# Performance work log

Measured on AMD Instinct MI355X. Metric: run time of the kernel, lower is better.

Reference implementation:

```python
import jax, jax.numpy as jnp
import numpy as np

INPUT_SIZE = 512.0
NMS_THRESH = 0.3
SCORE_THRESH = 0.5
TOPC = 256        # candidates entering NMS (top-scoring above-threshold boxes)
MAX_DETS = 32     # py_cpu_nms(...)[:32]


def conv3x3(x, w):
    return jax.lax.conv_general_dilated(x, w, (1, 1), 'SAME',
                                        dimension_numbers=('NCHW', 'OIHW', 'NCHW'))


def bn_eval(x, g, b, m, v, eps=1e-5):
    inv = g * jax.lax.rsqrt(v + eps)
    return x * inv[None, :, None, None] + (b - m * inv)[None, :, None, None]


def lrelu(x):
    return jnp.where(x >= 0, x, 0.01 * x)


def upsample2x(x):  # F.interpolate(scale_factor=2), default nearest
    return jnp.repeat(jnp.repeat(x, 2, axis=2), 2, axis=3)


def fpn_head(x, hw1, hg1, hb1, hm1, hv1, hw2, hg2, hb2, hm2, hv2):
    x = lrelu(bn_eval(conv3x3(x, hw1), hg1, hb1, hm1, hv1))
    x = lrelu(bn_eval(conv3x3(x, hw2), hg2, hb2, hm2, hv2))
    return x


def decode_boxes(t, a):
    # inverse of coordinate_change: x1 = ax1 + tx*aw, w = aw*exp(tw)
    aw = a[:, 2] - a[:, 0]
    ah = a[:, 3] - a[:, 1]
    x1 = a[:, 0] + t[:, 0] * aw
    y1 = a[:, 1] + t[:, 1] * ah
    bw = aw * jnp.exp(t[:, 2])
    bh = ah * jnp.exp(t[:, 3])
    return jnp.stack([x1, y1, x1 + bw, y1 + bh], axis=1)


def pairwise_iou_p1(b):
    # py_cpu_nms convention: +1 in widths/areas
    x1, y1, x2, y2 = b[:, 0], b[:, 1], b[:, 2], b[:, 3]
    areas = (x2 - x1 + 1.0) * (y2 - y1 + 1.0)
    xx1 = jnp.maximum(x1[:, None], x1[None, :])
    yy1 = jnp.maximum(y1[:, None], y1[None, :])
    xx2 = jnp.minimum(x2[:, None], x2[None, :])
    yy2 = jnp.minimum(y2[:, None], y2[None, :])
    inter = jnp.maximum(0.0, xx2 - xx1 + 1.0) * jnp.maximum(0.0, yy2 - yy1 + 1.0)
    return inter / (areas[:, None] + areas[None, :] - inter)


def nms_keep(boxes, valid):
    # boxes pre-sorted by descending score; greedy suppression
    ovr = pairwise_iou_p1(boxes)
    idxs = jnp.arange(boxes.shape[0])

    def body(i, keep):
        sup = (ovr[i] > NMS_THRESH) & (idxs > i) & keep[i]
        return keep & ~sup

    return jax.lax.fori_loop(0, boxes.shape[0], body, valid)


def roi_adaptive_maxpool(feat, c):
    # feat [C,h,w]; c = [x1,y1,x2,y2] int32 feature-map coords
    # faithful F.adaptive_max_pool2d(feat[:, y1:y2, x1:x2], (7,7))
    C, h, w = feat.shape
    neg = jnp.finfo(feat.dtype).min

    def bin_masks(lo, hi, n_axis):
        L = hi - lo
        i = jnp.arange(7)
        start = (i * L) // 7
        end = ((i + 1) * L + 6) // 7  # ceil
        rel = jnp.arange(n_axis) - lo
        return (rel[None, :] >= start[:, None]) & (rel[None, :] < end[:, None])

    my = bin_masks(c[1], c[3], h)  # [7,h]
    mx = bin_masks(c[0], c[2], w)  # [7,w]
    rows = jnp.stack([jnp.max(jnp.where(my[i][None, :, None], feat, neg), axis=1)
                      for i in range(7)])                    # [7y,C,w]
    cols = jnp.stack([jnp.max(jnp.where(mx[j][None, None, :], rows, neg), axis=2)
                      for j in range(7)])
    return cols.transpose(2, 1, 0)


def rpn_level(feat, anchors, stride, clsw, locw):
    B = feat.shape[0]
    score = jax.nn.sigmoid(conv3x3(feat, clsw)).transpose(0, 2, 3, 1).reshape(B, -1)
    loc = conv3x3(feat, locw).transpose(0, 2, 3, 1).reshape(B, -1, 4)

    def per_image(f, sc, t):
        boxes = jnp.clip(decode_boxes(t, anchors), 0.0, INPUT_SIZE)
        bw = boxes[:, 2] - boxes[:, 0]
        bh = boxes[:, 3] - boxes[:, 1]
        valid = (sc > SCORE_THRESH) & (bw >= 2.0 * stride) & (bh >= 2.0 * stride)
        vals, idx = jax.lax.top_k(jnp.where(valid, sc, -1.0), TOPC)
        cb = boxes[idx]
        # original NMS ran on detached numpy -> stop_gradient
        keep = nms_keep(jax.lax.stop_gradient(cb), vals > SCORE_THRESH)
        order = jnp.argsort(jnp.where(keep, 0, 1), stable=True)[:MAX_DETS]
        m = keep[order]
        b32 = cb[order]
        s32 = vals[order]
        coords = jnp.where(m[:, None], b32.astype(jnp.int32) // stride,
                           jnp.array([0, 0, 2, 2], jnp.int32))
        pooled = jax.vmap(lambda cc: roi_adaptive_maxpool(f, cc))(coords)
        pooled = jnp.where(m[:, None, None, None], pooled, 0.0)
        dets = jnp.where(m[:, None], jnp.concatenate([b32, s32[:, None]], axis=1), 0.0)
        return dets, m, pooled

    return jax.vmap(per_image)(feat, score, loc)


def net_forward(layer2, layer3, layer4, anchors2, anchors3, anchors4,
                hw1, hg1, hb1, hm1, hv1, hw2, hg2, hb2, hm2, hv2, clsw, locw):
    head = (hw1, hg1, hb1, hm1, hv1, hw2, hg2, hb2, hm2, hv2)
    l3 = layer3 + upsample2x(layer4)
    l2 = layer2 + upsample2x(l3)
    f2 = fpn_head(l2, *head)
    f3 = fpn_head(l3, *head)
    f4 = fpn_head(layer4, *head)
    outs = [rpn_level(f, a, s, clsw, locw)
            for f, a, s in ((f2, anchors2, 8), (f3, anchors3, 16), (f4, anchors4, 32))]
    dets = jnp.stack([o[0] for o in outs], axis=1)  # [B,3,32,5] padded eval_test
    mask = jnp.stack([o[1] for o in outs], axis=1)  # [B,3,32] validity of each det
    rois = jnp.stack([o[2] for o in outs], axis=1)  # [B,3,32,256,7,7]
    return dets, mask, rois


def setup_inputs() -> dict:
    key = jax.random.key(0)
    ks = jax.random.split(key, 16)
    f32 = jnp.float32

    def n(k, shape, s=1.0):
        return jax.random.normal(k, shape, f32) * s

    S = 512

    def anchors_for(st):
        h = S // st
        c = (jnp.arange(h, dtype=f32) + 0.5) * st
        sz = jnp.array([4.0, 6.0, 8.0], f32) * st
        cy = jnp.broadcast_to(c[:, None, None], (h, h, 3))
        cx = jnp.broadcast_to(c[None, :, None], (h, h, 3))
        ss = jnp.broadcast_to(sz[None, None, :], (h, h, 3))
        return jnp.stack([cx - ss / 2, cy - ss / 2, cx + ss / 2, cy + ss / 2], -1).reshape(-1, 4)

    return {
        'layer2': n(ks[0], (2, 256, 64, 64)),
        'layer3': n(ks[1], (2, 256, 32, 32)),
        'layer4': n(ks[2], (2, 256, 16, 16)),
        'anchors2': anchors_for(8),
        'anchors3': anchors_for(16),
        'anchors4': anchors_for(32),
        'hw1': n(ks[3], (256, 256, 3, 3), 0.03),
        'hg1': 1.0 + n(ks[4], (256,), 0.1),
        'hb1': n(ks[5], (256,), 0.1),
        'hm1': n(ks[6], (256,), 0.1),
        'hv1': jax.random.uniform(ks[7], (256,), f32, 0.5, 1.5),
        'hw2': n(ks[8], (256, 256, 3, 3), 0.03),
        'hg2': 1.0 + n(ks[9], (256,), 0.1),
        'hb2': n(ks[10], (256,), 0.1),
        'hm2': n(ks[11], (256,), 0.1),
        'hv2': jax.random.uniform(ks[12], (256,), f32, 0.5, 1.5),
        'clsw': n(ks[13], (3, 256, 3, 3), 0.03),
        'locw': n(ks[14], (12, 256, 3, 3), 0.01),
    }


def reference(layer2, layer3, layer4, anchors2, anchors3, anchors4,
              hw1, hg1, hb1, hm1, hv1, hw2, hg2, hb2, hm2, hv2, clsw, locw):
    return net_forward(layer2, layer3, layer4, anchors2, anchors3, anchors4,
                       hw1, hg1, hb1, hm1, hv1, hw2, hg2, hb2, hm2, hv2, clsw, locw)
```

## Files before the change

kernel.cpp:

```cpp
#include <hip/hip_runtime.h>
#include <math.h>

typedef __attribute__((ext_vector_type(8))) _Float16 f16x8;
typedef __attribute__((ext_vector_type(16))) float f32x16;
typedef unsigned long long ull;

__device__ __forceinline__ void split2(float v, _Float16& h, _Float16& l) {
  h = (_Float16)v;
  l = (_Float16)((v - (float)h) * 4096.0f);
}

#define OFF_W1H  0UL
#define OFF_W1L  1179648UL
#define OFF_W2H  2359296UL
#define OFF_W2L  3538944UL
#define OFF_WRH  4718592UL
#define OFF_WRL  4866048UL
#define OFF_I0H  5013504UL
#define OFF_I0L  9207808UL
#define OFF_I1H  13402112UL
#define OFF_I1L  14450688UL
#define OFF_I2H  15499264UL
#define OFF_I2L  15761408UL
#define OFF_L3F  16023552UL
#define OFF_H0H  18120704UL
#define OFF_H0L  22315008UL
#define OFF_H1H  26509312UL
#define OFF_H1L  27557888UL
#define OFF_H2H  28606464UL
#define OFF_H2L  28868608UL
#define OFF_LOGITS 29130752UL
#define OFF_TVALS  29259776UL
#define OFF_SKEY   29775872UL
#define OFF_COORDS 29904896UL
#define OFF_BN     29908992UL
#define OFF_HIST   29917184UL
#define OFF_P0     29966336UL
#define OFF_P1     40976384UL
#define WS_NEED    51986432UL


__global__ __launch_bounds__(256) void prep_bn_kernel(
    const float* __restrict__ hg1, const float* __restrict__ hb1,
    const float* __restrict__ hm1, const float* __restrict__ hv1,
    const float* __restrict__ hg2, const float* __restrict__ hb2,
    const float* __restrict__ hm2, const float* __restrict__ hv2,
    float* __restrict__ inv1, float* __restrict__ beta1,
    float* __restrict__ inv2, float* __restrict__ beta2)
{
  int t = threadIdx.x;
  float i1 = (float)((double)hg1[t] / sqrt((double)hv1[t] + 1e-5));
  inv1[t] = i1;
  beta1[t] = hb1[t] - hm1[t] * i1;
  float i2 = (float)((double)hg2[t] / sqrt((double)hv2[t] + 1e-5));
  inv2[t] = i2;
  beta2[t] = hb2[t] - hm2[t] * i2;
}

__global__ __launch_bounds__(256) void zero_hist_kernel(unsigned int* __restrict__ hist)
{
  hist[blockIdx.x * 256 + threadIdx.x] = 0u;
}

#define L1SZ 589824
#define RPNSZ 73728
__global__ __launch_bounds__(256) void prep_w_kernel(
    const float* __restrict__ hw1, const float* __restrict__ hw2,
    const float* __restrict__ clsw, const float* __restrict__ locw,
    char* __restrict__ ws)
{
  _Float16* w1h = (_Float16*)(ws + OFF_W1H);
  _Float16* w1l = (_Float16*)(ws + OFF_W1L);
  _Float16* w2h = (_Float16*)(ws + OFF_W2H);
  _Float16* w2l = (_Float16*)(ws + OFF_W2L);
  _Float16* wrh = (_Float16*)(ws + OFF_WRH);
  _Float16* wrl = (_Float16*)(ws + OFF_WRL);
  const int TOT = 2 * L1SZ + RPNSZ;
  for (int e = blockIdx.x * 256 + threadIdx.x; e < TOT; e += gridDim.x * 256) {
    float val; _Float16 *dh, *dl; int di;
    if (e < L1SZ) {
      int dydx = e >> 16, oc = (e >> 8) & 255, ic = e & 255;
      val = hw1[(size_t)(oc * 256 + ic) * 9 + dydx];
      dh = w1h; dl = w1l; di = e;
    } else if (e < 2 * L1SZ) {
      int e2 = e - L1SZ;
      int dydx = e2 >> 16, oc = (e2 >> 8) & 255, ic = e2 & 255;
      val = hw2[(size_t)(oc * 256 + ic) * 9 + dydx];
      dh = w2h; dl = w2l; di = e2;
    } else {
      int e3 = e - 2 * L1SZ;
      int dydx = e3 >> 13, oc = (e3 >> 8) & 31, ic = e3 & 255;
      if (oc < 3) val = clsw[(size_t)(oc * 256 + ic) * 9 + dydx];
      else if (oc < 15) val = locw[(size_t)((oc - 3) * 256 + ic) * 9 + dydx];
      else val = 0.f;
      dh = wrh; dl = wrl; di = e3;
    }
    _Float16 h, l;
    split2(val, h, l);
    dh[di] = h; dl[di] = l;
  }
}

__global__ __launch_bounds__(256) void fuse_kernel(
    const float* __restrict__ a, const float* __restrict__ bUp,
    float* __restrict__ f32chw, _Float16* __restrict__ oH, _Float16* __restrict__ oL,
    int H, int logW)
{
  __shared__ float T[32][65];
  int HW = H * H;
  int img = blockIdx.y;
  const float* ap = a + (size_t)img * 256 * HW;
  const float* bp = bUp ? (bUp + (size_t)img * 256 * (HW >> 2)) : nullptr;
  float* fp = f32chw ? (f32chw + (size_t)img * 256 * HW) : nullptr;
  _Float16* oHp = oH + (size_t)img * HW * 256;
  _Float16* oLp = oL + (size_t)img * HW * 256;
  int p0 = blockIdx.x * 64;
  int tid = threadIdx.x;
  int px = tid & 63, cg = tid >> 6;
  int gp = p0 + px;
  int y = gp >> logW, x = gp & (H - 1);
  int px2 = tid >> 2, q = tid & 3;
  for (int c0 = 0; c0 < 256; c0 += 32) {
    #pragma unroll
    for (int cc = 0; cc < 8; ++cc) {
      int c = c0 + cg * 8 + cc;
      float v = ap[(size_t)c * HW + gp];
      if (bp) v += bp[(size_t)c * (HW >> 2) + (y >> 1) * (H >> 1) + (x >> 1)];
      if (fp) fp[(size_t)c * HW + gp] = v;
      T[cg * 8 + cc][px] = v;
    }
    __syncthreads();
    {
      size_t oa = (size_t)(p0 + px2) * 256 + c0 + q * 8;
      f16x8 hs, ls;
      #pragma unroll
      for (int j = 0; j < 8; ++j) {
        float v = T[q * 8 + j][px2];
        _Float16 h, l;
        split2(v, h, l);
        hs[j] = h; ls[j] = l;
      }
      *(f16x8*)&oHp[oa] = hs;
      *(f16x8*)&oLp[oa] = ls;
    }
    __syncthreads();
  }
}

struct CArgs {
  const _Float16* inH[3]; const _Float16* inL[3];
  const _Float16* wH; const _Float16* wL;
  _Float16* outH[3]; _Float16* outL[3];
  const float* inv; const float* beta;
  float* logits; float* tvals;
  float* p0; float* p1;
  int mode; int parts;
};

template<int OCW, int WN, int NI>
__global__ __launch_bounds__(WN * 64, 2) void conv_mfma_kernel(CArgs a)
{
  constexpr int NT = WN * 64;
  constexpr int NOC = WN * NI * 32;
  __shared__ _Float16 Ph[2][4000], Pl[2][4000];

  int bt = blockIdx.x;
  int lvl, tile;
  if (bt < 64) { lvl = 0; tile = bt; }
  else if (bt < 80) { lvl = 1; tile = bt - 64; }
  else { lvl = 2; tile = bt - 80; }
  int H = (lvl == 0) ? 64 : ((lvl == 1) ? 32 : 16);
  int HW = H * H;
  int tpr = H >> 3;
  int ty0 = (tile / tpr) * 8, tx0 = (tile % tpr) * 8;
  int img = blockIdx.z;

  int part, ocb;
  if (a.parts == 1) { part = 0; ocb = blockIdx.y * NOC; }
  else if (OCW == 256) { part = blockIdx.y >> 1; ocb = (blockIdx.y & 1) * NOC; }
  else { part = blockIdx.y; ocb = 0; }
  int nicb = 8 / a.parts;
  int icb0 = part * nicb;
  float* pout = nullptr;
  if (a.parts == 2) pout = part ? a.p1 : a.p0;
  else if (a.parts == 4) pout = a.p0 + (size_t)part * 10752 * 32;

  const _Float16* inH = a.inH[lvl] + (size_t)img * HW * 256;
  const _Float16* inL = a.inL[lvl] + (size_t)img * HW * 256;

  int tid = threadIdx.x;
  int lane = tid & 63, wn = tid >> 6;
  int row = lane & 31, khalf = lane >> 5;
  int abase[2];
  #pragma unroll
  for (int mi = 0; mi < 2; ++mi) {
    int m = mi * 32 + row;
    abase[mi] = ((m >> 3) * 10 + (m & 7)) * 40 + khalf * 8;
  }

  const _Float16* wHb = a.wH + (size_t)(ocb + wn * NI * 32 + row) * 256 + khalf * 8 + icb0 * 32;
  const _Float16* wLb = a.wL + (size_t)(ocb + wn * NI * 32 + row) * 256 + khalf * 8 + icb0 * 32;

  f32x16 acc1[2][NI], acc2[2][NI];
  #pragma unroll
  for (int mi = 0; mi < 2; ++mi)
    #pragma unroll
    for (int ni = 0; ni < NI; ++ni)
      #pragma unroll
      for (int j = 0; j < 16; ++j) { acc1[mi][ni][j] = 0.f; acc2[mi][ni][j] = 0.f; }

  auto stage = [&](int icb, int buf) {
    for (int u = tid; u < 400; u += NT) {
      int pxl = u >> 2, icq = u & 3;
      int py = pxl / 10, pxx = pxl - py * 10;
      int gy = ty0 + py - 1, gx = tx0 + pxx - 1;
      int lo = pxl * 40 + icq * 8;
      if ((unsigned)gy < (unsigned)H && (unsigned)gx < (unsigned)H) {
        size_t ga = (size_t)(gy * H + gx) * 256 + icb * 32 + icq * 8;
        *(f16x8*)&Ph[buf][lo] = *(const f16x8*)&inH[ga];
        *(f16x8*)&Pl[buf][lo] = *(const f16x8*)&inL[ga];
      } else {
        f16x8 z;
        #pragma unroll
        for (int j = 0; j < 8; ++j) z[j] = (_Float16)0.f;
        *(f16x8*)&Ph[buf][lo] = z;
        *(f16x8*)&Pl[buf][lo] = z;
      }
    }
  };

  stage(icb0, 0);
  __syncthreads();

  for (int rel = 0; rel < nicb; ++rel) {
    int cur = rel & 1;
    if (rel < nicb - 1) stage(icb0 + rel + 1, cur ^ 1);
    #pragma unroll
    for (int dydx = 0; dydx < 9; ++dydx) {
      int sh = ((dydx / 3) * 10 + (dydx % 3)) * 40;
      #pragma unroll
      for (int k2 = 0; k2 < 2; ++k2) {
        f16x8 bh[NI], bl[NI], ah[2], al[2];
        #pragma unroll
        for (int ni = 0; ni < NI; ++ni) {
          size_t ga = (size_t)dydx * OCW * 256 + (size_t)ni * 32 * 256 + rel * 32 + k2 * 16;
          bh[ni] = *(const f16x8*)&wHb[ga];
          bl[ni] = *(const f16x8*)&wLb[ga];
        }
        #pragma unroll
        for (int mi = 0; mi < 2; ++mi) {
          int off = abase[mi] + sh + k2 * 16;
          ah[mi] = *(const f16x8*)&Ph[cur][off];
          al[mi] = *(const f16x8*)&Pl[cur][off];
        }
        #pragma unroll
        for (int mi = 0; mi < 2; ++mi)
          #pragma unroll
          for (int ni = 0; ni < NI; ++ni) {
            acc1[mi][ni] = __builtin_amdgcn_mfma_f32_32x32x16_f16(ah[mi], bh[ni], acc1[mi][ni], 0, 0, 0);
            acc2[mi][ni] = __builtin_amdgcn_mfma_f32_32x32x16_f16(ah[mi], bl[ni], acc2[mi][ni], 0, 0, 0);
            acc2[mi][ni] = __builtin_amdgcn_mfma_f32_32x32x16_f16(al[mi], bh[ni], acc2[mi][ni], 0, 0, 0);
          }
      }
    }
    __syncthreads();
  }

  int poffv = (lvl == 0) ? 0 : ((lvl == 1) ? 4096 : 5120);
  #pragma unroll
  for (int mi = 0; mi < 2; ++mi)
    #pragma unroll
    for (int ni = 0; ni < NI; ++ni) {
      int oc = ocb + wn * NI * 32 + ni * 32 + row;
      float v[16];
      #pragma unroll
      for (int r = 0; r < 16; ++r) v[r] = acc1[mi][ni][r] + acc2[mi][ni][r] * (1.f / 4096.f);
      if (pout) {
        float* pp = pout + (size_t)(img * 5376 + poffv) * OCW;
        #pragma unroll
        for (int r = 0; r < 16; ++r) {
          int ml = (r & 3) + 8 * (r >> 2) + 4 * khalf;
          int m = mi * 32 + ml;
          int y = ty0 + (m >> 3), x = tx0 + (m & 7);
          pp[(size_t)(y * H + x) * OCW + oc] = v[r];
        }
      } else if (a.mode == 0) {
        _Float16* outH = a.outH[lvl] + (size_t)img * HW * 256;
        _Float16* outL = a.outL[lvl] + (size_t)img * HW * 256;
        float iv = a.inv[oc], bb = a.beta[oc];
        #pragma unroll
        for (int r = 0; r < 16; ++r) {
          int ml = (r & 3) + 8 * (r >> 2) + 4 * khalf;
          int m = mi * 32 + ml;
          int y = ty0 + (m >> 3), x = tx0 + (m & 7);
          float vv = v[r] * iv + bb;
          vv = (vv >= 0.f) ? vv : 0.01f * vv;
          _Float16 h, l;
          split2(vv, h, l);
          size_t oa = (size_t)(y * H + x) * 256 + oc;
          outH[oa] = h;
          outL[oa] = l;
        }
      } else {
        if (oc < 15) {
          int abse = (lvl == 0) ? 0 : ((lvl == 1) ? 12288 : 15360);
          #pragma unroll
          for (int r = 0; r < 16; ++r) {
            int ml = (r & 3) + 8 * (r >> 2) + 4 * khalf;
            int m = mi * 32 + ml;
            int y = ty0 + (m >> 3), x = tx0 + (m & 7);
            int gi = img * 16128 + abse + (y * H + x) * 3;
            if (oc < 3) a.logits[gi + oc] = v[r];
            else { int r2 = oc - 3; a.tvals[(size_t)(gi + (r2 >> 2)) * 4 + (r2 & 3)] = v[r]; }
          }
        }
      }
    }
}

__global__ __launch_bounds__(256) void combine_head_kernel(
    const float* __restrict__ p0, const float* __restrict__ p1,
    const float* __restrict__ inv, const float* __restrict__ beta,
    _Float16* __restrict__ oH0, _Float16* __restrict__ oL0,
    _Float16* __restrict__ oH1, _Float16* __restrict__ oL1,
    _Float16* __restrict__ oH2, _Float16* __restrict__ oL2)
{
  int g = blockIdx.x * 256 + threadIdx.x;
  int pixel = g >> 5, q = g & 31;
  size_t base = (size_t)pixel * 256 + q * 8;
  int img = pixel / 5376, rem = pixel - img * 5376;
  int lvl = (rem < 4096) ? 0 : ((rem < 5120) ? 1 : 2);
  int poffv = (lvl == 0) ? 0 : ((lvl == 1) ? 4096 : 5120);
  int HW = (lvl == 0) ? 4096 : ((lvl == 1) ? 1024 : 256);
  int lpx = rem - poffv;
  size_t oa = ((size_t)img * HW + lpx) * 256 + q * 8;
  _Float16* oH = ((lvl == 0) ? oH0 : ((lvl == 1) ? oH1 : oH2)) + oa;
  _Float16* oL = ((lvl == 0) ? oL0 : ((lvl == 1) ? oL1 : oL2)) + oa;
  f16x8 hs, ls;
  #pragma unroll
  for (int j = 0; j < 8; ++j) {
    int oc = q * 8 + j;
    float vv = (p0[base + j] + p1[base + j]) * inv[oc] + beta[oc];
    vv = (vv >= 0.f) ? vv : 0.01f * vv;
    _Float16 h, l;
    split2(vv, h, l);
    hs[j] = h; ls[j] = l;
  }
  *(f16x8*)oH = hs;
  *(f16x8*)oL = ls;
}

__global__ __launch_bounds__(256) void combine_rpn_kernel(
    const float* __restrict__ praw, float* __restrict__ logits, float* __restrict__ tvals)
{
  int g = blockIdx.x * 256 + threadIdx.x;
  int px = g >> 4, oc = g & 15;
  if (oc == 15) return;
  float s = 0.f;
  #pragma unroll
  for (int p = 0; p < 4; ++p) s += praw[((size_t)p * 10752 + px) * 32 + oc];
  int img = px / 5376, rem = px - img * 5376;
  int lvl = (rem < 4096) ? 0 : ((rem < 5120) ? 1 : 2);
  int poffv = (lvl == 0) ? 0 : ((lvl == 1) ? 4096 : 5120);
  int abase = (lvl == 0) ? 0 : ((lvl == 1) ? 12288 : 15360);
  int gi = img * 16128 + abase + (rem - poffv) * 3;
  if (oc < 3) logits[gi + oc] = s;
  else { int r2 = oc - 3; tvals[(size_t)(gi + (r2 >> 2)) * 4 + (r2 & 3)] = s; }
}

__device__ __forceinline__ void decode_one(const float* __restrict__ anch,
                                           const float* __restrict__ tv, int i,
                                           float& x1, float& y1, float& x2, float& y2)
{
  float t0 = tv[i * 4 + 0], t1 = tv[i * 4 + 1], t2 = tv[i * 4 + 2], t3 = tv[i * 4 + 3];
  float a0 = anch[i * 4 + 0], a1 = anch[i * 4 + 1], a2 = anch[i * 4 + 2], a3 = anch[i * 4 + 3];
  float aw = a2 - a0, ah = a3 - a1;
  float xx = a0 + t0 * aw;
  float yy = a1 + t1 * ah;
  float bw = aw * expf(t2);
  float bh = ah * expf(t3);
  x1 = fminf(fmaxf(xx, 0.f), 512.f);
  y1 = fminf(fmaxf(yy, 0.f), 512.f);
  x2 = fminf(fmaxf(xx + bw, 0.f), 512.f);
  y2 = fminf(fmaxf(yy + bh, 0.f), 512.f);
}

__global__ __launch_bounds__(256) void score_kernel(
    const float* __restrict__ logits, const float* __restrict__ tvals,
    const float* __restrict__ anch0, const float* __restrict__ anch1, const float* __restrict__ anch2,
    unsigned int* __restrict__ skey, unsigned int* __restrict__ hist)
{
  int g = blockIdx.x * 256 + threadIdx.x;
  if (g >= 2 * 16128) return;
  int img = g / 16128, r = g - img * 16128;
  int lvl = (r < 12288) ? 0 : ((r < 15360) ? 1 : 2);
  int abase = (lvl == 0) ? 0 : ((lvl == 1) ? 12288 : 15360);
  int stride = (lvl == 0) ? 8 : ((lvl == 1) ? 16 : 32);
  const float* anch = (lvl == 0) ? anch0 : ((lvl == 1) ? anch1 : anch2);
  int i = r - abase;
  float lv = logits[g];
  float sc = 1.f / (1.f + expf(-lv));
  float x1, y1, x2, y2;
  decode_one(anch, tvals + (size_t)(img * 16128 + abase) * 4, i, x1, y1, x2, y2);
  float minsz = 2.0f * (float)stride;
  bool valid = (sc > 0.5f) && ((x2 - x1) >= minsz) && ((y2 - y1) >= minsz);
  unsigned int key = valid ? __float_as_uint(sc) : 0u;
  skey[g] = key;
  if (valid)
    atomicAdd(&hist[(img * 3 + lvl) * 2048 + ((key & 0xFFFFFFu) >> 13)], 1u);
}

__global__ __launch_bounds__(256) void postproc_kernel(
    const float* __restrict__ tvals,
    const float* __restrict__ anch0, const float* __restrict__ anch1, const float* __restrict__ anch2,
    const unsigned int* __restrict__ skey, const unsigned int* __restrict__ hist,
    float* __restrict__ dout, int* __restrict__ coords)
{
  int lvl = blockIdx.x, img = blockIdx.y;
  int N = (lvl == 0) ? 12288 : ((lvl == 1) ? 3072 : 768);
  int stride = (lvl == 0) ? 8 : ((lvl == 1) ? 16 : 32);
  int abase = (lvl == 0) ? 0 : ((lvl == 1) ? 12288 : 15360);
  const float* anch = (lvl == 0) ? anch0 : ((lvl == 1) ? anch1 : anch2);
  const float* tv = tvals + (size_t)(img * 16128 + abase) * 4;
  const unsigned int* sk = skey + img * 16128 + abase;
  int tx = threadIdx.x;

  __shared__ int tot[256];
  __shared__ int sh_bin, sh_V;
  __shared__ ull slist[1024];
  __shared__ int scnt;
  __shared__ ull skey64[256];
  __shared__ float bx0[256], bx1[256], bx2[256], bx3[256], bar[256], bsc[256];
  __shared__ ull colT[256][4];
  __shared__ ull kinit[4], kfin[4];
  __shared__ unsigned char bkeepArr[256];
  __shared__ int sel[32];

  const unsigned int* hp = hist + (img * 3 + lvl) * 2048;
  unsigned int hloc[8];
  #pragma unroll
  for (int j = 0; j < 8; ++j) hloc[j] = hp[tx * 8 + j];
  int sl[9]; sl[8] = 0;
  #pragma unroll
  for (int j = 7; j >= 0; --j) sl[j] = sl[j + 1] + (int)hloc[j];
  tot[tx] = sl[0];
  if (tx == 0) { sh_bin = 2048; scnt = 0; }
  __syncthreads();
  int T = 0;
  for (int b = 0; b < 256; ++b) T += (b > tx) ? tot[b] : 0;
  if (tx == 0) sh_V = T + sl[0];
  __syncthreads();
  int V = sh_V;
  int needed = (V < 256) ? V : 256;
  if (needed > 0) {
    #pragma unroll
    for (int j = 0; j < 8; ++j) {
      int suf = T + sl[j];
      int sufn = (j < 7) ? (T + sl[j + 1]) : T;
      if (suf >= needed && sufn < needed) sh_bin = tx * 8 + j;
    }
  }
  #pragma unroll
  for (int q = 0; q < 4; ++q) slist[tx + q * 256] = 0ull;
  __syncthreads();
  int Bstar = sh_bin;

  if (needed > 0) {
    const uint4* sk4 = (const uint4*)sk;
    for (int i4 = tx; i4 < (N >> 2); i4 += 256) {
      uint4 v4 = sk4[i4];
      unsigned int vv[4] = {v4.x, v4.y, v4.z, v4.w};
      #pragma unroll
      for (int q = 0; q < 4; ++q) {
        unsigned int v = vv[q];
        if (v != 0u && (int)((v & 0xFFFFFFu) >> 13) >= Bstar) {
          int p = atomicAdd(&scnt, 1);
          if (p < 1024)
            slist[p] = ((ull)v << 32) | (ull)(0xFFFFFFFFu - (unsigned)(i4 * 4 + q));
        }
      }
    }
  }
  __syncthreads();
  int M = scnt < 1024 ? scnt : 1024;

  skey64[tx] = 0ull;
  __syncthreads();
  for (int it = tx; it < M; it += 256) {
    ull K = slist[it];
    int rank = 0;
    for (int j = 0; j < M; ++j) rank += (slist[j] > K) ? 1 : 0;
    if (rank < 256) skey64[rank] = K;
  }
  __syncthreads();

  {
    ull key = skey64[tx];
    float x1 = 0.f, y1 = 0.f, x2 = 0.f, y2 = 0.f, sc = 0.f;
    if (key != 0ull) {
      sc = __uint_as_float((unsigned int)(key >> 32));
      int idx = (int)(0xFFFFFFFFu - (unsigned int)(key & 0xFFFFFFFFull));
      decode_one(anch, tv, idx, x1, y1, x2, y2);
    }
    bx0[tx] = x1; bx1[tx] = y1; bx2[tx] = x2; bx3[tx] = y2;
    bsc[tx] = sc;
    bar[tx] = (x2 - x1 + 1.f) * (y2 - y1 + 1.f);
    ull b = __ballot(sc > 0.5f);
    if ((tx & 63) == 0) kinit[tx >> 6] = b;
  }
  __syncthreads();

  {
    float xj1 = bx0[tx], yj1 = bx1[tx], xj2 = bx2[tx], yj2 = bx3[tx], aj = bar[tx];
    #pragma unroll
    for (int w = 0; w < 4; ++w) {
      ull rr = 0ull;
      int j0 = w * 64;
      int ie = (tx < j0 + 64) ? tx : (j0 + 64);
      for (int i = j0; i < ie; ++i) {
        float xx1 = fmaxf(xj1, bx0[i]);
        float yy1 = fmaxf(yj1, bx1[i]);
        float xx2 = fminf(xj2, bx2[i]);
        float yy2 = fminf(yj2, bx3[i]);
        float ww = fmaxf(0.f, xx2 - xx1 + 1.f);
        float hh = fmaxf(0.f, yy2 - yy1 + 1.f);
        float inter = ww * hh;
        float ovr = inter / (aj + bar[i] - inter);
        rr |= (ovr > 0.3f) ? (1ull << (i & 63)) : 0ull;
      }
      colT[tx][w] = rr;
    }
  }
  __syncthreads();

  if (tx < 64) {
    int l = tx;
    ull cm[4][4];
    #pragma unroll
    for (int c = 0; c < 4; ++c)
      #pragma unroll
      for (int w = 0; w < 4; ++w) cm[c][w] = colT[l + 64 * c][w];
    int av[4];
    #pragma unroll
    for (int c = 0; c < 4; ++c) av[c] = (int)((kinit[c] >> l) & 1ull);
    for (int cw = 0; cw < 4; ++cw) {
      ull rem = __ballot(av[cw] != 0);
      while (rem) {
        int ib = __builtin_ctzll(rem);
        #pragma unroll
        for (int c = 0; c < 4; ++c) {
          int sup = (int)((cm[c][cw] >> ib) & 1ull);
          av[c] &= sup ^ 1;
        }
        ull ready = __ballot(av[cw] != 0);
        rem = (ib == 63) ? 0ull : (ready & (~0ull << (ib + 1)));
      }
    }
    #pragma unroll
    for (int c = 0; c < 4; ++c) {
      ull bw = __ballot(av[c] != 0);
      if (l == 0) kfin[c] = bw;
      bkeepArr[l + 64 * c] = (unsigned char)av[c];
    }
  }
  __syncthreads();

  {
    int r = tx;
    int m = bkeepArr[r];
    int K = 0, before = 0;
    #pragma unroll
    for (int c = 0; c < 4; ++c) {
      int pc = __popcll(kfin[c]);
      K += pc;
      if (r >= (c + 1) * 64) before += pc;
      else if (r > c * 64) before += __popcll(kfin[c] & ((1ull << (r - c * 64)) - 1ull));
    }
    int rank = m ? before : (K + r - before);
    if (rank < 32) sel[rank] = r;
  }
  __syncthreads();

  if (tx < 32) {
    int r = sel[tx];
    int m = bkeepArr[r];
    int ob = (img * 3 + lvl) * 32 + tx;
    float d0 = 0.f, d1 = 0.f, d2 = 0.f, d3 = 0.f, d4 = 0.f;
    int c0 = 0, c1 = 0, c2 = 2, c3 = 2;
    if (m) {
      d0 = bx0[r]; d1 = bx1[r]; d2 = bx2[r]; d3 = bx3[r]; d4 = bsc[r];
      c0 = ((int)d0) / stride; c1 = ((int)d1) / stride;
      c2 = ((int)d2) / stride; c3 = ((int)d3) / stride;
    }
    dout[ob * 5 + 0] = d0; dout[ob * 5 + 1] = d1; dout[ob * 5 + 2] = d2;
    dout[ob * 5 + 3] = d3; dout[ob * 5 + 4] = d4;
    dout[960 + ob] = m ? 1.f : 0.f;
    coords[ob * 5 + 0] = c0; coords[ob * 5 + 1] = c1;
    coords[ob * 5 + 2] = c2; coords[ob * 5 + 3] = c3;
    coords[ob * 5 + 4] = m;
  }
}

__global__ __launch_bounds__(256) void roipool_kernel(
    const _Float16* __restrict__ fh0, const _Float16* __restrict__ fl0,
    const _Float16* __restrict__ fh1, const _Float16* __restrict__ fl1,
    const _Float16* __restrict__ fh2, const _Float16* __restrict__ fl2,
    const int* __restrict__ coords, float* __restrict__ dout)
{
  int bx = blockIdx.x;
  int slot = bx / 49, bin = bx - slot * 49;
  int yi = bin / 7, xi = bin - yi * 7;
  int lvl = blockIdx.y, img = blockIdx.z;
  int ob = (img * 3 + lvl) * 32 + slot;
  int c = threadIdx.x;
  const int* cw = coords + ob * 5;
  float* outp = dout + 1152 + (size_t)ob * 256 * 49 + (size_t)c * 49 + yi * 7 + xi;
  int m = cw[4];
  if (!m) { *outp = 0.f; return; }
  int H = (lvl == 0) ? 64 : ((lvl == 1) ? 32 : 16);
  const _Float16* fh = ((lvl == 0) ? fh0 : ((lvl == 1) ? fh1 : fh2)) + (size_t)img * H * H * 256;
  const _Float16* fl = ((lvl == 0) ? fl0 : ((lvl == 1) ? fl1 : fl2)) + (size_t)img * H * H * 256;
  int lox = cw[0], loy = cw[1], hix = cw[2], hiy = cw[3];
  int Lx = hix - lox, Ly = hiy - loy;
  int ys = loy + (yi * Ly) / 7;
  int ye = loy + ((yi + 1) * Ly + 6) / 7;
  int xs = lox + (xi * Lx) / 7;
  int xe = lox + ((xi + 1) * Lx + 6) / 7;
  float mx = -3.402823466e+38f;
  for (int y = ys; y < ye; ++y) {
    size_t rowb = ((size_t)y * H) * 256 + c;
    for (int x = xs; x < xe; ++x) {
      size_t idx = rowb + (size_t)x * 256;
      float v = (float)fh[idx] + (float)fl[idx] * (1.f / 4096.f);
      mx = fmaxf(mx, v);
    }
  }
  *outp = mx;
}

extern "C" void kernel_launch(void* const* d_in, const int* in_sizes, int n_in,
                              void* d_out, int out_size, void* d_ws, size_t ws_size,
                              hipStream_t stream)
{
  (void)in_sizes; (void)n_in; (void)out_size;
  char* ws = (char*)d_ws;
  const float* layer2 = (const float*)d_in[0];
  const float* layer3 = (const float*)d_in[1];
  const float* layer4 = (const float*)d_in[2];
  const float* anch2  = (const float*)d_in[3];
  const float* anch3  = (const float*)d_in[4];
  const float* anch4  = (const float*)d_in[5];
  const float* hw1 = (const float*)d_in[6];
  const float* hg1 = (const float*)d_in[7];
  const float* hb1 = (const float*)d_in[8];
  const float* hm1 = (const float*)d_in[9];
  const float* hv1 = (const float*)d_in[10];
  const float* hw2 = (const float*)d_in[11];
  const float* hg2 = (const float*)d_in[12];
  const float* hb2 = (const float*)d_in[13];
  const float* hm2 = (const float*)d_in[14];
  const float* hv2 = (const float*)d_in[15];
  const float* clsw = (const float*)d_in[16];
  const float* locw = (const float*)d_in[17];
  float* dout = (float*)d_out;
  bool split = ws_size >= WS_NEED;

  _Float16* i0H = (_Float16*)(ws + OFF_I0H);
  _Float16* i0L = (_Float16*)(ws + OFF_I0L);
  _Float16* i1H = (_Float16*)(ws + OFF_I1H);
  _Float16* i1L = (_Float16*)(ws + OFF_I1L);
  _Float16* i2H = (_Float16*)(ws + OFF_I2H);
  _Float16* i2L = (_Float16*)(ws + OFF_I2L);
  float* l3f = (float*)(ws + OFF_L3F);
  _Float16* h0H = (_Float16*)(ws + OFF_H0H);
  _Float16* h0L = (_Float16*)(ws + OFF_H0L);
  _Float16* h1H = (_Float16*)(ws + OFF_H1H);
  _Float16* h1L = (_Float16*)(ws + OFF_H1L);
  _Float16* h2H = (_Float16*)(ws + OFF_H2H);
  _Float16* h2L = (_Float16*)(ws + OFF_H2L);
  float* logits = (float*)(ws + OFF_LOGITS);
  float* tvals  = (float*)(ws + OFF_TVALS);
  unsigned int* skey = (unsigned int*)(ws + OFF_SKEY);
  int* coords = (int*)(ws + OFF_COORDS);
  float* bn = (float*)(ws + OFF_BN);
  float* inv1 = bn; float* beta1 = bn + 256; float* inv2 = bn + 512; float* beta2 = bn + 768;
  unsigned int* hist = (unsigned int*)(ws + OFF_HIST);
  float* P0 = (float*)(ws + OFF_P0);
  float* P1 = (float*)(ws + OFF_P1);

  prep_bn_kernel<<<1, 256, 0, stream>>>(hg1, hb1, hm1, hv1, hg2, hb2, hm2, hv2,
                                        inv1, beta1, inv2, beta2);
  zero_hist_kernel<<<48, 256, 0, stream>>>(hist);
  prep_w_kernel<<<2048, 256, 0, stream>>>(hw1, hw2, clsw, locw, ws);

  fuse_kernel<<<dim3(4, 2), 256, 0, stream>>>(layer4, nullptr, nullptr, i2H, i2L, 16, 4);
  fuse_kernel<<<dim3(16, 2), 256, 0, stream>>>(layer3, layer4, l3f, i1H, i1L, 32, 5);
  fuse_kernel<<<dim3(64, 2), 256, 0, stream>>>(layer2, l3f, nullptr, i0H, i0L, 64, 6);

  CArgs c1;
  c1.inH[0] = i0H; c1.inH[1] = i1H; c1.inH[2] = i2H;
  c1.inL[0] = i0L; c1.inL[1] = i1L; c1.inL[2] = i2L;
  c1.wH = (const _Float16*)(ws + OFF_W1H); c1.wL = (const _Float16*)(ws + OFF_W1L);
  c1.outH[0] = h0H; c1.outH[1] = h1H; c1.outH[2] = h2H;
  c1.outL[0] = h0L; c1.outL[1] = h1L; c1.outL[2] = h2L;
  c1.inv = inv1; c1.beta = beta1;
  c1.logits = nullptr; c1.tvals = nullptr;
  c1.p0 = P0; c1.p1 = P1;
  c1.mode = 0; c1.parts = split ? 2 : 1;
  conv_mfma_kernel<256, 2, 2><<<dim3(84, split ? 4 : 2, 2), 128, 0, stream>>>(c1);
  if (split)
    combine_head_kernel<<<1344, 256, 0, stream>>>(P0, P1, inv1, beta1,
                                                  h0H, h0L, h1H, h1L, h2H, h2L);

  _Float16* f0H = i0H; _Float16* f0L = i0L;
  _Float16* f1H = i1H; _Float16* f1L = i1L;
  _Float16* f2H = i2H; _Float16* f2L = i2L;

  CArgs c2;
  c2.inH[0] = h0H; c2.inH[1] = h1H; c2.inH[2] = h2H;
  c2.inL[0] = h0L; c2.inL[1] = h1L; c2.inL[2] = h2L;
  c2.wH = (const _Float16*)(ws + OFF_W2H); c2.wL = (const _Float16*)(ws + OFF_W2L);
  c2.outH[0] = f0H; c2.outH[1] = f1H; c2.outH[2] = f2H;
  c2.outL[0] = f0L; c2.outL[1] = f1L; c2.outL[2] = f2L;
  c2.inv = inv2; c2.beta = beta2;
  c2.logits = nullptr; c2.tvals = nullptr;
  c2.p0 = P0; c2.p1 = P1;
  c2.mode = 0; c2.parts = split ? 2 : 1;
  conv_mfma_kernel<256, 2, 2><<<dim3(84, split ? 4 : 2, 2), 128, 0, stream>>>(c2);
  if (split)
    combine_head_kernel<<<1344, 256, 0, stream>>>(P0, P1, inv2, beta2,
                                                  f0H, f0L, f1H, f1L, f2H, f2L);

  CArgs cr;
  cr.inH[0] = f0H; cr.inH[1] = f1H; cr.inH[2] = f2H;
  cr.inL[0] = f0L; cr.inL[1] = f1L; cr.inL[2] = f2L;
  cr.wH = (const _Float16*)(ws + OFF_WRH); cr.wL = (const _Float16*)(ws + OFF_WRL);
  cr.outH[0] = nullptr; cr.outH[1] = nullptr; cr.outH[2] = nullptr;
  cr.outL[0] = nullptr; cr.outL[1] = nullptr; cr.outL[2] = nullptr;
  cr.inv = nullptr; cr.beta = nullptr;
  cr.logits = logits; cr.tvals = tvals;
  cr.p0 = P1; cr.p1 = nullptr;
  cr.mode = 2; cr.parts = split ? 4 : 1;
  conv_mfma_kernel<32, 1, 1><<<dim3(84, split ? 4 : 1, 2), 64, 0, stream>>>(cr);
  if (split)
    combine_rpn_kernel<<<672, 256, 0, stream>>>(P1, logits, tvals);

  score_kernel<<<126, 256, 0, stream>>>(logits, tvals, anch2, anch3, anch4, skey, hist);
  postproc_kernel<<<dim3(3, 2), 256, 0, stream>>>(tvals, anch2, anch3, anch4, skey, hist, dout, coords);
  roipool_kernel<<<dim3(32 * 49, 3, 2), 256, 0, stream>>>(f0H, f0L, f1H, f1L, f2H, f2L, coords, dout);
}
```

Baseline: 322.5 us.

## Generalize split-K partials to 4/8 parts and pad LDS pixel stride

```diff
diff --git a/kernel.cpp b/kernel.cpp
--- a/kernel.cpp
+++ b/kernel.cpp
@@ -36,8 +36,9 @@
 #define OFF_BN     29908992UL
 #define OFF_HIST   29917184UL
 #define OFF_P0     29966336UL
-#define OFF_P1     40976384UL
-#define WS_NEED    51986432UL
+#define PSLOT      11010048UL
+#define WS_NEED2   51986432UL
+#define WS_NEED4   74006528UL
 
 
 __global__ __launch_bounds__(256) void prep_bn_kernel(
@@ -153,16 +154,19 @@
   _Float16* outH[3]; _Float16* outL[3];
   const float* inv; const float* beta;
   float* logits; float* tvals;
-  float* p0; float* p1;
+  float* pbase; size_t pstride;
   int mode; int parts;
 };
 
+#define PXS 42
+
 template<int OCW, int WN, int NI>
 __global__ __launch_bounds__(WN * 64, 2) void conv_mfma_kernel(CArgs a)
 {
   constexpr int NT = WN * 64;
   constexpr int NOC = WN * NI * 32;
-  __shared__ _Float16 Ph[2][4000], Pl[2][4000];
+  constexpr int OCG = OCW / NOC;
+  __shared__ _Float16 Ph[2][100 * PXS], Pl[2][100 * PXS];
 
   int bt = blockIdx.x;
   int lvl, tile;
@@ -175,15 +179,11 @@
   int ty0 = (tile / tpr) * 8, tx0 = (tile % tpr) * 8;
   int img = blockIdx.z;
 
-  int part, ocb;
-  if (a.parts == 1) { part = 0; ocb = blockIdx.y * NOC; }
-  else if (OCW == 256) { part = blockIdx.y >> 1; ocb = (blockIdx.y & 1) * NOC; }
-  else { part = blockIdx.y; ocb = 0; }
+  int part = blockIdx.y / OCG;
+  int ocb = (blockIdx.y % OCG) * NOC;
   int nicb = 8 / a.parts;
   int icb0 = part * nicb;
-  float* pout = nullptr;
-  if (a.parts == 2) pout = part ? a.p1 : a.p0;
-  else if (a.parts == 4) pout = a.p0 + (size_t)part * 10752 * 32;
+  float* pout = (a.parts > 1) ? (a.pbase + (size_t)part * a.pstride) : nullptr;
 
   const _Float16* inH = a.inH[lvl] + (size_t)img * HW * 256;
   const _Float16* inL = a.inL[lvl] + (size_t)img * HW * 256;
@@ -195,7 +195,7 @@
   #pragma unroll
   for (int mi = 0; mi < 2; ++mi) {
     int m = mi * 32 + row;
-    abase[mi] = ((m >> 3) * 10 + (m & 7)) * 40 + khalf * 8;
+    abase[mi] = ((m >> 3) * 10 + (m & 7)) * PXS + khalf * 8;
   }
 
   const _Float16* wHb = a.wH + (size_t)(ocb + wn * NI * 32 + row) * 256 + khalf * 8 + icb0 * 32;
@@ -214,7 +214,7 @@
       int pxl = u >> 2, icq = u & 3;
       int py = pxl / 10, pxx = pxl - py * 10;
       int gy = ty0 + py - 1, gx = tx0 + pxx - 1;
-      int lo = pxl * 40 + icq * 8;
+      int lo = pxl * PXS + icq * 8;
       if ((unsigned)gy < (unsigned)H && (unsigned)gx < (unsigned)H) {
         size_t ga = (size_t)(gy * H + gx) * 256 + icb * 32 + icq * 8;
         *(f16x8*)&Ph[buf][lo] = *(const f16x8*)&inH[ga];
@@ -237,7 +237,7 @@
     if (rel < nicb - 1) stage(icb0 + rel + 1, cur ^ 1);
     #pragma unroll
     for (int dydx = 0; dydx < 9; ++dydx) {
-      int sh = ((dydx / 3) * 10 + (dydx % 3)) * 40;
+      int sh = ((dydx / 3) * 10 + (dydx % 3)) * PXS;
       #pragma unroll
       for (int k2 = 0; k2 < 2; ++k2) {
         f16x8 bh[NI], bl[NI], ah[2], al[2];
@@ -319,12 +319,13 @@
 }
 
 __global__ __launch_bounds__(256) void combine_head_kernel(
-    const float* __restrict__ p0, const float* __restrict__ p1,
+    const float* __restrict__ pb, int nparts,
     const float* __restrict__ inv, const float* __restrict__ beta,
     _Float16* __restrict__ oH0, _Float16* __restrict__ oL0,
     _Float16* __restrict__ oH1, _Float16* __restrict__ oL1,
     _Float16* __restrict__ oH2, _Float16* __restrict__ oL2)
 {
+  const size_t PS = 10752UL * 256UL;
   int g = blockIdx.x * 256 + threadIdx.x;
   int pixel = g >> 5, q = g & 31;
   size_t base = (size_t)pixel * 256 + q * 8;
@@ -340,7 +341,9 @@
   #pragma unroll
   for (int j = 0; j < 8; ++j) {
     int oc = q * 8 + j;
-    float vv = (p0[base + j] + p1[base + j]) * inv[oc] + beta[oc];
+    float s = 0.f;
+    for (int k = 0; k < nparts; ++k) s += pb[(size_t)k * PS + base + j];
+    float vv = s * inv[oc] + beta[oc];
     vv = (vv >= 0.f) ? vv : 0.01f * vv;
     _Float16 h, l;
     split2(vv, h, l);
@@ -351,14 +354,14 @@
 }
 
 __global__ __launch_bounds__(256) void combine_rpn_kernel(
-    const float* __restrict__ praw, float* __restrict__ logits, float* __restrict__ tvals)
+    const float* __restrict__ praw, int nparts,
+    float* __restrict__ logits, float* __restrict__ tvals)
 {
   int g = blockIdx.x * 256 + threadIdx.x;
   int px = g >> 4, oc = g & 15;
   if (oc == 15) return;
   float s = 0.f;
-  #pragma unroll
-  for (int p = 0; p < 4; ++p) s += praw[((size_t)p * 10752 + px) * 32 + oc];
+  for (int p = 0; p < nparts; ++p) s += praw[((size_t)p * 10752 + px) * 32 + oc];
   int img = px / 5376, rem = px - img * 5376;
   int lvl = (rem < 4096) ? 0 : ((rem < 5120) ? 1 : 2);
   int poffv = (lvl == 0) ? 0 : ((lvl == 1) ? 4096 : 5120);
@@ -663,7 +666,9 @@
   const float* clsw = (const float*)d_in[16];
   const float* locw = (const float*)d_in[17];
   float* dout = (float*)d_out;
-  bool split = ws_size >= WS_NEED;
+
+  int hparts = (ws_size >= WS_NEED4) ? 4 : ((ws_size >= WS_NEED2) ? 2 : 1);
+  int rparts = (ws_size >= WS_NEED2) ? 8 : 1;
 
   _Float16* i0H = (_Float16*)(ws + OFF_I0H);
   _Float16* i0L = (_Float16*)(ws + OFF_I0L);
@@ -686,7 +691,6 @@
   float* inv1 = bn; float* beta1 = bn + 256; float* inv2 = bn + 512; float* beta2 = bn + 768;
   unsigned int* hist = (unsigned int*)(ws + OFF_HIST);
   float* P0 = (float*)(ws + OFF_P0);
-  float* P1 = (float*)(ws + OFF_P1);
 
   prep_bn_kernel<<<1, 256, 0, stream>>>(hg1, hb1, hm1, hv1, hg2, hb2, hm2, hv2,
                                         inv1, beta1, inv2, beta2);
@@ -705,11 +709,11 @@
   c1.outL[0] = h0L; c1.outL[1] = h1L; c1.outL[2] = h2L;
   c1.inv = inv1; c1.beta = beta1;
   c1.logits = nullptr; c1.tvals = nullptr;
-  c1.p0 = P0; c1.p1 = P1;
-  c1.mode = 0; c1.parts = split ? 2 : 1;
-  conv_mfma_kernel<256, 2, 2><<<dim3(84, split ? 4 : 2, 2), 128, 0, stream>>>(c1);
-  if (split)
-    combine_head_kernel<<<1344, 256, 0, stream>>>(P0, P1, inv1, beta1,
+  c1.pbase = P0; c1.pstride = 10752UL * 256UL;
+  c1.mode = 0; c1.parts = hparts;
+  conv_mfma_kernel<256, 2, 2><<<dim3(84, hparts * 2, 2), 128, 0, stream>>>(c1);
+  if (hparts > 1)
+    combine_head_kernel<<<1344, 256, 0, stream>>>(P0, hparts, inv1, beta1,
                                                   h0H, h0L, h1H, h1L, h2H, h2L);
 
   _Float16* f0H = i0H; _Float16* f0L = i0L;
@@ -724,11 +728,11 @@
   c2.outL[0] = f0L; c2.outL[1] = f1L; c2.outL[2] = f2L;
   c2.inv = inv2; c2.beta = beta2;
   c2.logits = nullptr; c2.tvals = nullptr;
-  c2.p0 = P0; c2.p1 = P1;
-  c2.mode = 0; c2.parts = split ? 2 : 1;
-  conv_mfma_kernel<256, 2, 2><<<dim3(84, split ? 4 : 2, 2), 128, 0, stream>>>(c2);
-  if (split)
-    combine_head_kernel<<<1344, 256, 0, stream>>>(P0, P1, inv2, beta2,
+  c2.pbase = P0; c2.pstride = 10752UL * 256UL;
+  c2.mode = 0; c2.parts = hparts;
+  conv_mfma_kernel<256, 2, 2><<<dim3(84, hparts * 2, 2), 128, 0, stream>>>(c2);
+  if (hparts > 1)
+    combine_head_kernel<<<1344, 256, 0, stream>>>(P0, hparts, inv2, beta2,
                                                   f0H, f0L, f1H, f1L, f2H, f2L);
 
   CArgs cr;
@@ -739,11 +743,11 @@
   cr.outL[0] = nullptr; cr.outL[1] = nullptr; cr.outL[2] = nullptr;
   cr.inv = nullptr; cr.beta = nullptr;
   cr.logits = logits; cr.tvals = tvals;
-  cr.p0 = P1; cr.p1 = nullptr;
-  cr.mode = 2; cr.parts = split ? 4 : 1;
-  conv_mfma_kernel<32, 1, 1><<<dim3(84, split ? 4 : 1, 2), 64, 0, stream>>>(cr);
-  if (split)
-    combine_rpn_kernel<<<672, 256, 0, stream>>>(P1, logits, tvals);
+  cr.pbase = P0; cr.pstride = 10752UL * 32UL;
+  cr.mode = 2; cr.parts = rparts;
+  conv_mfma_kernel<32, 1, 1><<<dim3(84, rparts, 2), 64, 0, stream>>>(cr);
+  if (rparts > 1)
+    combine_rpn_kernel<<<672, 256, 0, stream>>>(P0, rparts, logits, tvals);
 
   score_kernel<<<126, 256, 0, stream>>>(logits, tvals, anch2, anch3, anch4, skey, hist);
   postproc_kernel<<<dim3(3, 2), 256, 0, stream>>>(tvals, anch2, anch3, anch4, skey, hist, dout, coords);
```

Result: slower. 462.6 us (+43.4%).
